# Optimization experiments

Measured on AMD Instinct MI355X. Metric: run time of the kernel, lower is better.

The kernel has to match this reference:

```python
import jax, jax.numpy as jnp
import numpy as np

MARGIN = 0.5
EPS = 1e-5
NOISE_RATE = 0.5


def setup_inputs() -> dict:
    key = jax.random.key(0)
    k1, k2, k3, k4, k5 = jax.random.split(key, 5)
    n, m, d, c = 1024, 65536, 512, 10000
    return {
        "inputs_col": jax.random.normal(k1, (n, d), dtype=jnp.float32),
        "inputs_row": jax.random.normal(k2, (m, d), dtype=jnp.float32),
        "center": jax.random.normal(k3, (c, d), dtype=jnp.float32),
        "targets_col": jax.random.randint(k4, (n,), 0, c, dtype=jnp.int64),
        "target_row": jax.random.randint(k5, (m,), 0, c, dtype=jnp.int64),
        "filled_mask": jnp.ones((c,), dtype=bool),
    }


def _prism_keep(features, targets, center, filled_mask, noise_rate):
    # no_grad in the original -> stop_gradient here
    f = jax.lax.stop_gradient(features)
    c = jax.lax.stop_gradient(center)
    # all_sim_exp[cls] / sum(all_sim_exp) is exactly softmax over class logits
    probs = jax.nn.softmax(f @ c.T, axis=-1)          # [n, num_classes]
    sel = jnp.take_along_axis(probs, targets[:, None], axis=1)[:, 0]  # [n]
    C = jnp.where(filled_mask[targets], sel, 1.0)      # not-in-memory -> 1
    n = C.shape[0]
    n_remove = int(noise_rate * n)                     # static
    to_remove = jnp.argsort(C)[:n_remove]
    # empty margin_window path: keep everything except to_remove
    keep = jnp.ones((n,), dtype=bool).at[to_remove].set(False)
    return keep


def reference(inputs_col, inputs_row, center, targets_col, target_row, filled_mask):
    n = inputs_col.shape[0]
    sim = inputs_col @ inputs_row.T                    # [n, m]
    pos_mask = targets_col[:, None] == target_row[None, :]
    neg_mask = (~pos_mask) & (sim > MARGIN)
    pos_mask = pos_mask & (sim < 1.0 - EPS)

    keep = _prism_keep(inputs_col, targets_col, center, filled_mask, NOISE_RATE)
    pos_mask = pos_mask & keep[:, None]
    neg_mask = neg_mask & keep[:, None]

    # sum over selected pairs without boolean-indexing (masked reductions)
    pos_loss = jnp.sum(jnp.where(pos_mask, 1.0 - sim, 0.0))
    neg_loss = jnp.sum(jnp.where(neg_mask, sim, 0.0))
    loss = (pos_loss + neg_loss) / n
    return loss, keep
```

## Files before the change

### kernel.cpp

```cpp
#include <hip/hip_runtime.h>


typedef int    v4i   __attribute__((ext_vector_type(4)));
typedef float  f32x4 __attribute__((ext_vector_type(4)));
typedef unsigned char u8;

#define N_COL  1024
#define M_ROW  65536
#define DDIM   512
#define NCLS   10000
#define NT     79
#define NREM   512

#define OFF_A8   0u
#define OFF_C8   524288u
#define OFF_B8   5701632u
#define OFF_PMS  39256064u
#define OFF_LT   39903232u
#define OFF_COMP 39907328u
#define OFF_TCC  39909376u
#define OFF_ACC  39911424u
#define OFF_CNT  39911432u

__device__ __forceinline__ void async16(const void* g, void* l) {
    __builtin_amdgcn_global_load_lds(
        (const __attribute__((address_space(1))) void*)g,
        (__attribute__((address_space(3))) void*)l, 16, 0, 0);
}

__device__ __forceinline__ unsigned pack4_fp8(float4 v) {
    int r = 0;
    r = __builtin_amdgcn_cvt_pk_fp8_f32(v.x, v.y, r, false);
    r = __builtin_amdgcn_cvt_pk_fp8_f32(v.z, v.w, r, true);
    return (unsigned)r;
}

__device__ __forceinline__ void gemm8_128(const u8* __restrict__ A,
                                          const u8* __restrict__ B,
                                          int m0, int n0,
                                          u8* As, u8* Bs, f32x4 (&acc)[4][4]) {
    const int tid = threadIdx.x, wid = tid >> 6, lane = tid & 63;
    const int wm = wid >> 1, wn = wid & 1;
    const int q = lane >> 4, lc = lane & 15;

    const u8* gA[4]; const u8* gB[4]; int voff[4];
#pragma unroll
    for (int s = 0; s < 4; ++s) {
        const int c  = wid * 256 + s * 64 + lane;
        const int r  = c >> 3;
        const int gs = (c & 7) ^ (r & 7);
        gA[s] = A + (size_t)(m0 + r) * DDIM + gs * 16;
        gB[s] = B + (size_t)(n0 + r) * DDIM + gs * 16;
        voff[s] = c * 16;
    }
#pragma unroll
    for (int i = 0; i < 4; ++i)
#pragma unroll
        for (int j = 0; j < 4; ++j) acc[i][j] = (f32x4){0.f, 0.f, 0.f, 0.f};

    for (int kt = 0; kt < 4; ++kt) {
        const int kb = kt * 128;
#pragma unroll
        for (int s = 0; s < 4; ++s) {
            async16(gA[s] + kb, As + voff[s]);
            async16(gB[s] + kb, Bs + voff[s]);
        }
        __syncthreads();
#pragma unroll
        for (int ks = 0; ks < 4; ++ks) {
            const int gg = ks * 2 + (q >> 1);
            const int bo = (q & 1) * 8;
            long long af[4], bv[4];
#pragma unroll
            for (int i = 0; i < 4; ++i) {
                const int rA = wm * 64 + i * 16 + lc;
                af[i] = *(const long long*)(As + (rA * 8 + (gg ^ (rA & 7))) * 16 + bo);
                const int rB = wn * 64 + i * 16 + lc;
                bv[i] = *(const long long*)(Bs + (rB * 8 + (gg ^ (rB & 7))) * 16 + bo);
            }
#pragma unroll
            for (int i = 0; i < 4; ++i)
#pragma unroll
                for (int j = 0; j < 4; ++j)
                    acc[i][j] = __builtin_amdgcn_mfma_f32_16x16x32_fp8_fp8(
                        af[i], bv[j], acc[i][j], 0, 0, 0);
        }
        __syncthreads();
    }
}

__global__ void k_prep(const float4* __restrict__ a4, const float4* __restrict__ c4,
                       const float* __restrict__ a32, const float* __restrict__ c32,
                       const int* __restrict__ tcol,
                       unsigned* __restrict__ A8w, uint2* __restrict__ C8w,
                       float* __restrict__ lt, double* __restrict__ accd,
                       unsigned* __restrict__ cnt) {
    const int b = blockIdx.x, tid = threadIdx.x;
    if (b == 0 && tid == 0) { *accd = 0.0; *cnt = 0u; }
    if (b < 256) {
        const int idx = b * 256 + tid;
        A8w[idx * 2]     = pack4_fp8(a4[idx * 2]);
        A8w[idx * 2 + 1] = pack4_fp8(a4[idx * 2 + 1]);
    } else if (b < 2784) {
        const int cidx = (b - 256) * 256 + tid;
        const int row  = cidx >> 6;
        uint2 o = make_uint2(0u, 0u);
        if (row < NCLS) {
            o.x = pack4_fp8(c4[cidx * 2]);
            o.y = pack4_fp8(c4[cidx * 2 + 1]);
        }
        C8w[cidx] = o;
    } else {
        const int w = (b - 2784) * 4 + (tid >> 6), lane = tid & 63;
        const int t = tcol[w];
        const float* ar = a32 + (size_t)w * DDIM;
        const float* cr = c32 + (size_t)t * DDIM;
        float s = 0.f;
#pragma unroll
        for (int k = 0; k < DDIM / 64; ++k) s += ar[lane + k * 64] * cr[lane + k * 64];
        for (int off = 32; off; off >>= 1) s += __shfl_down(s, off, 64);
        if (lane == 0) lt[w] = s;
    }
}

__global__ __launch_bounds__(256, 3) void k_mid(const u8* __restrict__ A8,
                                                const u8* __restrict__ C8,
                                                const float4* __restrict__ brow4,
                                                uint2* __restrict__ B8v,
                                                float2* __restrict__ pms) {
    const int b = blockIdx.x, tid = threadIdx.x;
    if (b < 632) {
        __shared__ __align__(16) u8 As[16384], Bs[16384];
        __shared__ float s_mm[128][2], s_ss[128][2];
        const int n_t = b >> 3, m0 = (b & 7) * 128, n0 = n_t * 128;
        f32x4 acc[4][4];
        gemm8_128(A8, C8, m0, n0, As, Bs, acc);

        const int wid = tid >> 6, lane = tid & 63;
        const int wm = wid >> 1, wn = wid & 1, q = lane >> 4, lc = lane & 15;
        const int cbase = n0 + wn * 64 + lc;
#pragma unroll
        for (int i = 0; i < 4; ++i) {
#pragma unroll
            for (int reg = 0; reg < 4; ++reg) {
                float mm = -INFINITY, ss = 0.f;
#pragma unroll
                for (int j = 0; j < 4; ++j)
                    if (cbase + j * 16 < NCLS) mm = fmaxf(mm, acc[i][j][reg]);
#pragma unroll
                for (int j = 0; j < 4; ++j)
                    if (cbase + j * 16 < NCLS) ss += __expf(acc[i][j][reg] - mm);
#pragma unroll
                for (int d2 = 1; d2 < 16; d2 <<= 1) {
                    float mo = __shfl_xor(mm, d2, 16);
                    float so = __shfl_xor(ss, d2, 16);
                    float M = fmaxf(mm, mo), S = 0.f;
                    if (ss > 0.f) S += ss * __expf(mm - M);
                    if (so > 0.f) S += so * __expf(mo - M);
                    mm = M; ss = S;
                }
                if (lc == 0) {
                    const int row = i * 16 + q * 4 + reg;
                    s_mm[wm * 64 + row][wn] = mm;
                    s_ss[wm * 64 + row][wn] = ss;
                }
            }
        }
        __syncthreads();
        if (tid < 128) {
            float m1 = s_mm[tid][0], s1 = s_ss[tid][0];
            float m2 = s_mm[tid][1], s2 = s_ss[tid][1];
            float M = fmaxf(m1, m2), S = 0.f;
            if (s1 > 0.f) S += s1 * __expf(m1 - M);
            if (s2 > 0.f) S += s2 * __expf(m2 - M);
            pms[(size_t)n_t * N_COL + m0 + tid] = make_float2(M, S);
        }
    } else {
        int idx = (b - 632) * 256 + tid;
#pragma unroll
        for (int it = 0; it < 4; ++it, idx += 1048576) {
            B8v[idx] = make_uint2(pack4_fp8(brow4[idx * 2]),
                                  pack4_fp8(brow4[idx * 2 + 1]));
        }
    }
}

__global__ __launch_bounds__(1024) void k_sel(const float2* __restrict__ pms,
                                              const float* __restrict__ lt,
                                              const int* __restrict__ tcol,
                                              int* __restrict__ comp,
                                              int* __restrict__ tcc,
                                              float* __restrict__ keep_out) {
    __shared__ float v[N_COL];
    const int i = threadIdx.x;
    float M = -INFINITY, S = 0.f;
    for (int t = 0; t < NT; ++t) {
        float2 p = pms[(size_t)t * N_COL + i];
        if (p.y > 0.f) {
            if (p.x > M) { S = S * __expf(M - p.x) + p.y; M = p.x; }
            else         { S += p.y * __expf(p.x - M); }
        }
    }
    const float x = lt[i] - (M + logf(S));
    v[i] = x;
    __syncthreads();
    int rank = 0;
    const float4* v4 = (const float4*)v;
#pragma unroll 8
    for (int j4 = 0; j4 < N_COL / 4; ++j4) {
        float4 w = v4[j4];
        const int j = j4 * 4;
        rank += (w.x < x) || (w.x == x && j     < i);
        rank += (w.y < x) || (w.y == x && j + 1 < i);
        rank += (w.z < x) || (w.z == x && j + 2 < i);
        rank += (w.w < x) || (w.w == x && j + 3 < i);
    }
    const bool keep = rank >= NREM;
    keep_out[i] = keep ? 1.0f : 0.0f;
    if (keep) { comp[rank - NREM] = i; tcc[rank - NREM] = tcol[i]; }
}

__global__ __launch_bounds__(512, 2) void k_loss(const u8* __restrict__ A8,
                                                 const u8* __restrict__ B8,
                                                 const int* __restrict__ comp,
                                                 const int* __restrict__ tcc,
                                                 const int* __restrict__ trow,
                                                 double* __restrict__ accd,
                                                 unsigned* __restrict__ cnt,
                                                 float* __restrict__ out) {
    __shared__ __align__(16) u8 As[32768], Bs[16384];
    __shared__ int s_map[256], s_tc[256], s_tr[128];
    __shared__ float s_red[8];
    const int b = blockIdx.x, tid = threadIdx.x;
    const int xcd = b & 7, l = b >> 3;
    const int n0 = (xcd * 64 + (l >> 1)) * 128;
    const int m0 = (l & 1) * 256;
    if (tid < 256)      { s_map[tid] = comp[m0 + tid]; s_tc[tid] = tcc[m0 + tid]; }
    else if (tid < 384) { s_tr[tid - 256] = trow[n0 + tid - 256]; }
    __syncthreads();

    const int wid = tid >> 6, lane = tid & 63;
    const int wm = wid >> 1, wn = wid & 1;
    const int q = lane >> 4, lc = lane & 15;

    const u8* gA[4]; int vA[4]; const u8* gB[2]; int vB[2];
#pragma unroll
    for (int s = 0; s < 4; ++s) {
        const int c  = wid * 512 + s * 64 + lane;
        const int cc = s * 512 + tid;
        const int r  = cc >> 3, gs = (cc & 7) ^ (r & 7);
        gA[s] = A8 + (size_t)s_map[r] * DDIM + gs * 16;
        vA[s] = cc * 16;
        (void)c;
    }
#pragma unroll
    for (int s = 0; s < 2; ++s) {
        const int cc = s * 512 + tid;
        const int r  = cc >> 3, gs = (cc & 7) ^ (r & 7);
        gB[s] = B8 + (size_t)(n0 + r) * DDIM + gs * 16;
        vB[s] = cc * 16;
    }

    f32x4 acc[4][4];
#pragma unroll
    for (int i = 0; i < 4; ++i)
#pragma unroll
        for (int j = 0; j < 4; ++j) acc[i][j] = (f32x4){0.f, 0.f, 0.f, 0.f};

    for (int kt = 0; kt < 4; ++kt) {
        const int kb = kt * 128;
#pragma unroll
        for (int s = 0; s < 4; ++s) async16(gA[s] + kb, As + vA[s]);
#pragma unroll
        for (int s = 0; s < 2; ++s) async16(gB[s] + kb, Bs + vB[s]);
        __syncthreads();
#pragma unroll
        for (int ks = 0; ks < 4; ++ks) {
            const int gg = ks * 2 + (q >> 1);
            const int bo = (q & 1) * 8;
            long long af[4], bv[4];
#pragma unroll
            for (int i = 0; i < 4; ++i) {
                const int rA = wm * 64 + i * 16 + lc;
                af[i] = *(const long long*)(As + (rA * 8 + (gg ^ (rA & 7))) * 16 + bo);
                const int rB = wn * 64 + i * 16 + lc;
                bv[i] = *(const long long*)(Bs + (rB * 8 + (gg ^ (rB & 7))) * 16 + bo);
            }
#pragma unroll
            for (int i = 0; i < 4; ++i)
#pragma unroll
                for (int j = 0; j < 4; ++j)
                    acc[i][j] = __builtin_amdgcn_mfma_f32_16x16x32_fp8_fp8(
                        af[i], bv[j], acc[i][j], 0, 0, 0);
        }
        __syncthreads();
    }

    const float POSMAX = 1.0f - 1e-5f;
    float local = 0.f;
#pragma unroll
    for (int i = 0; i < 4; ++i) {
#pragma unroll
        for (int j = 0; j < 4; ++j) {
            const int tr = s_tr[wn * 64 + j * 16 + lc];
#pragma unroll
            for (int reg = 0; reg < 4; ++reg) {
                const int row = wm * 64 + i * 16 + q * 4 + reg;
                const float sim = acc[i][j][reg];
                if (s_tc[row] == tr) {
                    if (sim < POSMAX) local += 1.0f - sim;
                } else if (sim > 0.5f) {
                    local += sim;
                }
            }
        }
    }
    for (int off = 32; off; off >>= 1) local += __shfl_down(local, off, 64);
    if (lane == 0) s_red[wid] = local;
    __syncthreads();
    if (tid == 0) {
        float blk = 0.f;
#pragma unroll
        for (int w = 0; w < 8; ++w) blk += s_red[w];
        atomicAdd(accd, (double)blk);
        __threadfence();
        if (atomicAdd(cnt, 1u) == 1023u) {
            double vfin = atomicAdd(accd, 0.0);
            out[0] = (float)(vfin / (double)N_COL);
        }
    }
}

extern "C" void kernel_launch(void* const* d_in, const int* in_sizes, int n_in,
                              void* d_out, int out_size, void* d_ws, size_t ws_size,
                              hipStream_t stream) {
    (void)in_sizes; (void)n_in; (void)out_size; (void)ws_size;
    const float* inputs_col  = (const float*)d_in[0];
    const float* inputs_row  = (const float*)d_in[1];
    const float* center      = (const float*)d_in[2];
    const int*   targets_col = (const int*)d_in[3];
    const int*   target_row  = (const int*)d_in[4];
    float* out = (float*)d_out;
    char*  ws  = (char*)d_ws;

    u8*       A8   = (u8*)(ws + OFF_A8);
    u8*       C8   = (u8*)(ws + OFF_C8);
    u8*       B8   = (u8*)(ws + OFF_B8);
    float2*   pms  = (float2*)(ws + OFF_PMS);
    float*    lt   = (float*) (ws + OFF_LT);
    int*      comp = (int*)   (ws + OFF_COMP);
    int*      tcc  = (int*)   (ws + OFF_TCC);
    double*   accd = (double*)(ws + OFF_ACC);
    unsigned* cnt  = (unsigned*)(ws + OFF_CNT);

    k_prep<<<3040, 256, 0, stream>>>((const float4*)inputs_col, (const float4*)center,
                                     inputs_col, center, targets_col,
                                     (unsigned*)A8, (uint2*)C8, lt, accd, cnt);
    k_mid<<<4728, 256, 0, stream>>>(A8, C8, (const float4*)inputs_row,
                                    (uint2*)B8, pms);
    k_sel<<<1, 1024, 0, stream>>>(pms, lt, targets_col, comp, tcc, out + 1);
    k_loss<<<1024, 512, 0, stream>>>(A8, B8, comp, tcc, target_row, accd, cnt, out);
}
```

Measured before the change: 346.8 us.

## Fuse fp32-to-fp8 row conversion into loss GEMM with double-buffered K loop

The separate pass that converted inputs_row to fp8 and stored it in workspace is removed from k_mid. k_loss now loads fp32 rows directly, packs them to fp8 in registers and writes them to LDS. Each block now covers all 512 kept columns for its 128 rows, using 64-wide K steps and double-buffered LDS. This removes the 32MB fp8 write and the repeated fp8 reads of B, in exchange for larger LDS use, 128 accumulator registers per thread, and synchronous fp32 global loads in the main loop.

```diff
diff --git a/kernel.cpp b/kernel.cpp
--- a/kernel.cpp
+++ b/kernel.cpp
@@ -14,7 +14,6 @@
 
 #define OFF_A8   0u
 #define OFF_C8   524288u
-#define OFF_B8   5701632u
 #define OFF_PMS  39256064u
 #define OFF_LT   39903232u
 #define OFF_COMP 39907328u
@@ -125,63 +124,52 @@
 
 __global__ __launch_bounds__(256, 3) void k_mid(const u8* __restrict__ A8,
                                                 const u8* __restrict__ C8,
-                                                const float4* __restrict__ brow4,
-                                                uint2* __restrict__ B8v,
                                                 float2* __restrict__ pms) {
     const int b = blockIdx.x, tid = threadIdx.x;
-    if (b < 632) {
-        __shared__ __align__(16) u8 As[16384], Bs[16384];
-        __shared__ float s_mm[128][2], s_ss[128][2];
-        const int n_t = b >> 3, m0 = (b & 7) * 128, n0 = n_t * 128;
-        f32x4 acc[4][4];
-        gemm8_128(A8, C8, m0, n0, As, Bs, acc);
-
-        const int wid = tid >> 6, lane = tid & 63;
-        const int wm = wid >> 1, wn = wid & 1, q = lane >> 4, lc = lane & 15;
-        const int cbase = n0 + wn * 64 + lc;
-#pragma unroll
-        for (int i = 0; i < 4; ++i) {
-#pragma unroll
-            for (int reg = 0; reg < 4; ++reg) {
-                float mm = -INFINITY, ss = 0.f;
-#pragma unroll
-                for (int j = 0; j < 4; ++j)
-                    if (cbase + j * 16 < NCLS) mm = fmaxf(mm, acc[i][j][reg]);
-#pragma unroll
-                for (int j = 0; j < 4; ++j)
-                    if (cbase + j * 16 < NCLS) ss += __expf(acc[i][j][reg] - mm);
-#pragma unroll
-                for (int d2 = 1; d2 < 16; d2 <<= 1) {
-                    float mo = __shfl_xor(mm, d2, 16);
-                    float so = __shfl_xor(ss, d2, 16);
-                    float M = fmaxf(mm, mo), S = 0.f;
-                    if (ss > 0.f) S += ss * __expf(mm - M);
-                    if (so > 0.f) S += so * __expf(mo - M);
-                    mm = M; ss = S;
-                }
-                if (lc == 0) {
-                    const int row = i * 16 + q * 4 + reg;
-                    s_mm[wm * 64 + row][wn] = mm;
-                    s_ss[wm * 64 + row][wn] = ss;
-                }
-            }
-        }
-        __syncthreads();
-        if (tid < 128) {
-            float m1 = s_mm[tid][0], s1 = s_ss[tid][0];
-            float m2 = s_mm[tid][1], s2 = s_ss[tid][1];
-            float M = fmaxf(m1, m2), S = 0.f;
-            if (s1 > 0.f) S += s1 * __expf(m1 - M);
-            if (s2 > 0.f) S += s2 * __expf(m2 - M);
-            pms[(size_t)n_t * N_COL + m0 + tid] = make_float2(M, S);
-        }
-    } else {
-        int idx = (b - 632) * 256 + tid;
-#pragma unroll
-        for (int it = 0; it < 4; ++it, idx += 1048576) {
-            B8v[idx] = make_uint2(pack4_fp8(brow4[idx * 2]),
-                                  pack4_fp8(brow4[idx * 2 + 1]));
-        }
+    __shared__ __align__(16) u8 As[16384], Bs[16384];
+    __shared__ float s_mm[128][2], s_ss[128][2];
+    const int n_t = b >> 3, m0 = (b & 7) * 128, n0 = n_t * 128;
+    f32x4 acc[4][4];
+    gemm8_128(A8, C8, m0, n0, As, Bs, acc);
+
+    const int wid = tid >> 6, lane = tid & 63;
+    const int wm = wid >> 1, wn = wid & 1, q = lane >> 4, lc = lane & 15;
+    const int cbase = n0 + wn * 64 + lc;
+#pragma unroll
+    for (int i = 0; i < 4; ++i) {
+#pragma unroll
+        for (int reg = 0; reg < 4; ++reg) {
+            float mm = -INFINITY, ss = 0.f;
+#pragma unroll
+            for (int j = 0; j < 4; ++j)
+                if (cbase + j * 16 < NCLS) mm = fmaxf(mm, acc[i][j][reg]);
+#pragma unroll
+            for (int j = 0; j < 4; ++j)
+                if (cbase + j * 16 < NCLS) ss += __expf(acc[i][j][reg] - mm);
+#pragma unroll
+            for (int d2 = 1; d2 < 16; d2 <<= 1) {
+                float mo = __shfl_xor(mm, d2, 16);
+                float so = __shfl_xor(ss, d2, 16);
+                float M = fmaxf(mm, mo), S = 0.f;
+                if (ss > 0.f) S += ss * __expf(mm - M);
+                if (so > 0.f) S += so * __expf(mo - M);
+                mm = M; ss = S;
+            }
+            if (lc == 0) {
+                const int row = i * 16 + q * 4 + reg;
+                s_mm[wm * 64 + row][wn] = mm;
+                s_ss[wm * 64 + row][wn] = ss;
+            }
+        }
+    }
+    __syncthreads();
+    if (tid < 128) {
+        float m1 = s_mm[tid][0], s1 = s_ss[tid][0];
+        float m2 = s_mm[tid][1], s2 = s_ss[tid][1];
+        float M = fmaxf(m1, m2), S = 0.f;
+        if (s1 > 0.f) S += s1 * __expf(m1 - M);
+        if (s2 > 0.f) S += s2 * __expf(m2 - M);
+        pms[(size_t)n_t * N_COL + m0 + tid] = make_float2(M, S);
     }
 }
 
@@ -221,91 +209,111 @@
 }
 
 __global__ __launch_bounds__(512, 2) void k_loss(const u8* __restrict__ A8,
-                                                 const u8* __restrict__ B8,
+                                                 const float4* __restrict__ brow4,
                                                  const int* __restrict__ comp,
                                                  const int* __restrict__ tcc,
                                                  const int* __restrict__ trow,
                                                  double* __restrict__ accd,
                                                  unsigned* __restrict__ cnt,
                                                  float* __restrict__ out) {
-    __shared__ __align__(16) u8 As[32768], Bs[16384];
-    __shared__ int s_map[256], s_tc[256], s_tr[128];
+    __shared__ __align__(16) u8 As[2][32768];
+    __shared__ __align__(16) u8 Bs[2][8192];
+    __shared__ int s_map[512], s_tc[512], s_tr[128];
     __shared__ float s_red[8];
     const int b = blockIdx.x, tid = threadIdx.x;
-    const int xcd = b & 7, l = b >> 3;
-    const int n0 = (xcd * 64 + (l >> 1)) * 128;
-    const int m0 = (l & 1) * 256;
-    if (tid < 256)      { s_map[tid] = comp[m0 + tid]; s_tc[tid] = tcc[m0 + tid]; }
-    else if (tid < 384) { s_tr[tid - 256] = trow[n0 + tid - 256]; }
+    const int n0 = b * 128;
+    s_map[tid] = comp[tid];
+    s_tc[tid]  = tcc[tid];
+    if (tid < 128) s_tr[tid] = trow[n0 + tid];
     __syncthreads();
 
     const int wid = tid >> 6, lane = tid & 63;
     const int wm = wid >> 1, wn = wid & 1;
     const int q = lane >> 4, lc = lane & 15;
 
-    const u8* gA[4]; int vA[4]; const u8* gB[2]; int vB[2];
+    const u8* gA[4]; int vA[4];
 #pragma unroll
     for (int s = 0; s < 4; ++s) {
-        const int c  = wid * 512 + s * 64 + lane;
         const int cc = s * 512 + tid;
-        const int r  = cc >> 3, gs = (cc & 7) ^ (r & 7);
+        const int r  = cc >> 2, gs = (cc & 3) ^ (r & 3);
         gA[s] = A8 + (size_t)s_map[r] * DDIM + gs * 16;
         vA[s] = cc * 16;
-        (void)c;
-    }
-#pragma unroll
-    for (int s = 0; s < 2; ++s) {
-        const int cc = s * 512 + tid;
-        const int r  = cc >> 3, gs = (cc & 7) ^ (r & 7);
-        gB[s] = B8 + (size_t)(n0 + r) * DDIM + gs * 16;
-        vB[s] = cc * 16;
-    }
-
-    f32x4 acc[4][4];
-#pragma unroll
-    for (int i = 0; i < 4; ++i)
+    }
+    const int rB0 = tid >> 2, gB0 = tid & 3;
+    const float4* gB = brow4 + (size_t)(n0 + rB0) * (DDIM / 4) + gB0 * 4;
+    const int vB = (rB0 * 4 + (gB0 ^ (rB0 & 3))) * 16;
+
+    f32x4 acc[8][4];
+#pragma unroll
+    for (int i = 0; i < 8; ++i)
 #pragma unroll
         for (int j = 0; j < 4; ++j) acc[i][j] = (f32x4){0.f, 0.f, 0.f, 0.f};
 
-    for (int kt = 0; kt < 4; ++kt) {
-        const int kb = kt * 128;
-#pragma unroll
-        for (int s = 0; s < 4; ++s) async16(gA[s] + kb, As + vA[s]);
-#pragma unroll
-        for (int s = 0; s < 2; ++s) async16(gB[s] + kb, Bs + vB[s]);
-        __syncthreads();
-#pragma unroll
-        for (int ks = 0; ks < 4; ++ks) {
+    auto compute = [&](const u8* Asc, const u8* Bsc) {
+#pragma unroll
+        for (int ks = 0; ks < 2; ++ks) {
             const int gg = ks * 2 + (q >> 1);
             const int bo = (q & 1) * 8;
-            long long af[4], bv[4];
-#pragma unroll
-            for (int i = 0; i < 4; ++i) {
-                const int rA = wm * 64 + i * 16 + lc;
-                af[i] = *(const long long*)(As + (rA * 8 + (gg ^ (rA & 7))) * 16 + bo);
-                const int rB = wn * 64 + i * 16 + lc;
-                bv[i] = *(const long long*)(Bs + (rB * 8 + (gg ^ (rB & 7))) * 16 + bo);
-            }
-#pragma unroll
-            for (int i = 0; i < 4; ++i)
+            long long af[8], bv[4];
+#pragma unroll
+            for (int i = 0; i < 8; ++i) {
+                const int rA = wm * 128 + i * 16 + lc;
+                af[i] = *(const long long*)(Asc + (rA * 4 + (gg ^ (rA & 3))) * 16 + bo);
+            }
+#pragma unroll
+            for (int j = 0; j < 4; ++j) {
+                const int rB = wn * 64 + j * 16 + lc;
+                bv[j] = *(const long long*)(Bsc + (rB * 4 + (gg ^ (rB & 3))) * 16 + bo);
+            }
+#pragma unroll
+            for (int i = 0; i < 8; ++i)
 #pragma unroll
                 for (int j = 0; j < 4; ++j)
                     acc[i][j] = __builtin_amdgcn_mfma_f32_16x16x32_fp8_fp8(
                         af[i], bv[j], acc[i][j], 0, 0, 0);
         }
+    };
+
+    {
+#pragma unroll
+        for (int s = 0; s < 4; ++s) async16(gA[s], As[0] + vA[s]);
+        float4 f0 = gB[0], f1 = gB[1], f2 = gB[2], f3 = gB[3];
+        uint4 pk;
+        pk.x = pack4_fp8(f0); pk.y = pack4_fp8(f1);
+        pk.z = pack4_fp8(f2); pk.w = pack4_fp8(f3);
+        *(uint4*)(Bs[0] + vB) = pk;
         __syncthreads();
     }
+    int cur = 0;
+    for (int kt = 0; kt < 7; ++kt) {
+        const int nxt = cur ^ 1;
+        const int kb  = (kt + 1) * 64;
+#pragma unroll
+        for (int s = 0; s < 4; ++s) async16(gA[s] + kb, As[nxt] + vA[s]);
+        const float4* gb = gB + (size_t)(kt + 1) * 16;
+        float4 f0 = gb[0], f1 = gb[1], f2 = gb[2], f3 = gb[3];
+
+        compute(As[cur], Bs[cur]);
+
+        uint4 pk;
+        pk.x = pack4_fp8(f0); pk.y = pack4_fp8(f1);
+        pk.z = pack4_fp8(f2); pk.w = pack4_fp8(f3);
+        *(uint4*)(Bs[nxt] + vB) = pk;
+        __syncthreads();
+        cur = nxt;
+    }
+    compute(As[cur], Bs[cur]);
 
     const float POSMAX = 1.0f - 1e-5f;
     float local = 0.f;
 #pragma unroll
-    for (int i = 0; i < 4; ++i) {
+    for (int i = 0; i < 8; ++i) {
 #pragma unroll
         for (int j = 0; j < 4; ++j) {
             const int tr = s_tr[wn * 64 + j * 16 + lc];
 #pragma unroll
             for (int reg = 0; reg < 4; ++reg) {
-                const int row = wm * 64 + i * 16 + q * 4 + reg;
+                const int row = wm * 128 + i * 16 + q * 4 + reg;
                 const float sim = acc[i][j][reg];
                 if (s_tc[row] == tr) {
                     if (sim < POSMAX) local += 1.0f - sim;
@@ -324,7 +332,7 @@
         for (int w = 0; w < 8; ++w) blk += s_red[w];
         atomicAdd(accd, (double)blk);
         __threadfence();
-        if (atomicAdd(cnt, 1u) == 1023u) {
+        if (atomicAdd(cnt, 1u) == 511u) {
             double vfin = atomicAdd(accd, 0.0);
             out[0] = (float)(vfin / (double)N_COL);
         }
@@ -345,7 +353,6 @@
 
     u8*       A8   = (u8*)(ws + OFF_A8);
     u8*       C8   = (u8*)(ws + OFF_C8);
-    u8*       B8   = (u8*)(ws + OFF_B8);
     float2*   pms  = (float2*)(ws + OFF_PMS);
     float*    lt   = (float*) (ws + OFF_LT);
     int*      comp = (int*)   (ws + OFF_COMP);
@@ -356,8 +363,8 @@
     k_prep<<<3040, 256, 0, stream>>>((const float4*)inputs_col, (const float4*)center,
                                      inputs_col, center, targets_col,
                                      (unsigned*)A8, (uint2*)C8, lt, accd, cnt);
-    k_mid<<<4728, 256, 0, stream>>>(A8, C8, (const float4*)inputs_row,
-                                    (uint2*)B8, pms);
+    k_mid<<<632, 256, 0, stream>>>(A8, C8, pms);
     k_sel<<<1, 1024, 0, stream>>>(pms, lt, targets_col, comp, tcc, out + 1);
-    k_loss<<<1024, 512, 0, stream>>>(A8, B8, comp, tcc, target_row, accd, cnt, out);
-}
+    k_loss<<<512, 512, 0, stream>>>(A8, (const float4*)inputs_row,
+                                    comp, tcc, target_row, accd, cnt, out);
+}
```

New measurement: 332.4 us. -4.2%, faster.
